# Performance work log

Measured on AMD Instinct MI355X. Metric: run time of the kernel, lower is better.

The kernel has to match this reference:

```python
import jax, jax.numpy as jnp
import numpy as np

VOCAB = 100000
PAD_ID = VOCAB - 2
INTEREST_ID = VOCAB - 1


def setup_inputs() -> dict:
    key = jax.random.key(0)
    k1, k2, k3 = jax.random.split(key, 3)
    B, S, H = 1024, 200, 128
    hidden_states = jax.random.normal(k1, (B, S, H), dtype=jnp.float32)
    input_ids = jax.random.randint(k2, (B, S), 0, VOCAB, dtype=jnp.int64)
    w_proj = jax.random.normal(k3, (H,), dtype=jnp.float32) * (1.0 / np.sqrt(H))
    b_proj = jnp.zeros((1,), dtype=jnp.float32)
    return {"hidden_states": hidden_states, "input_ids": input_ids,
            "w_proj": w_proj, "b_proj": b_proj}


def reference(hidden_states, input_ids, w_proj, b_proj):
    # hidden_states: [B, S, H]; input_ids: [B, S]
    B, S, H = hidden_states.shape
    mask = (input_ids != PAD_ID) & (input_ids != INTEREST_ID)  # [B, S]
    # additive attention: queries = hidden, keys = first token state
    keys = hidden_states[:, 0:1, :]                 # [B, 1, H]
    features = jnp.tanh(hidden_states + keys)       # [B, S, H]
    scores = jnp.einsum('bsh,h->bs', features, w_proj) + b_proj[0]
    scores = jnp.where(mask, scores, -jnp.inf)
    attention_weights = jax.nn.softmax(scores, axis=-1)  # [B, S]
    # scatter-add attention weights into vocab-sized output (duplicate ids accumulate)
    batch_idx = jnp.arange(B)[:, None]              # [B, 1]
    repeat_probs = jnp.zeros((B, VOCAB), dtype=hidden_states.dtype)
    repeat_probs = repeat_probs.at[batch_idx, input_ids].add(attention_weights)
    return repeat_probs
```

## Files before the change

### kernel.cpp

```cpp
#include <hip/hip_runtime.h>
#include <math.h>

#define B_          1024
#define S_          200
#define H_          128
#define VOCAB_      100000
#define PAD_ID_     99998
#define INTEREST_ID_ 99999

__global__ __launch_bounds__(256) void repeat_decoder_kernel(
    const float* __restrict__ hs,
    const int*   __restrict__ ids,
    const float* __restrict__ w,
    const float* __restrict__ bp,
    float*       __restrict__ out)
{
    __shared__ float s_scores[S_];
    __shared__ float s_red[8];

    const int batch = blockIdx.x;
    const int tid   = threadIdx.x;
    const int wave  = tid >> 6;
    const int lane  = tid & 63;

    const float* hsb = hs + (size_t)batch * (S_ * H_);

    const float2 key = ((const float2*)hsb)[lane];
    const float2 wv  = ((const float2*)w)[lane];

    for (int s = wave; s < S_; s += 4) {
        const float2 x = ((const float2*)(hsb + s * H_))[lane];
        float acc = tanhf(x.x + key.x) * wv.x + tanhf(x.y + key.y) * wv.y;
        #pragma unroll
        for (int off = 32; off; off >>= 1)
            acc += __shfl_down(acc, off, 64);
        if (lane == 0) s_scores[s] = acc;
    }
    __syncthreads();

    const float bias = bp[0];
    int   id    = 0;
    bool  valid = false;
    float sc    = -INFINITY;
    if (tid < S_) {
        id    = ids[batch * S_ + tid];
        valid = (id != PAD_ID_) && (id != INTEREST_ID_);
        sc    = valid ? (s_scores[tid] + bias) : -INFINITY;
    }

    float m = sc;
    #pragma unroll
    for (int off = 32; off; off >>= 1)
        m = fmaxf(m, __shfl_down(m, off, 64));
    if (lane == 0) s_red[wave] = m;
    __syncthreads();
    m = fmaxf(fmaxf(s_red[0], s_red[1]), fmaxf(s_red[2], s_red[3]));

    const float e = (tid < S_ && valid) ? expf(sc - m) : 0.0f;
    float t = e;
    #pragma unroll
    for (int off = 32; off; off >>= 1)
        t += __shfl_down(t, off, 64);
    if (lane == 0) s_red[4 + wave] = t;
    __syncthreads();
    const float sum = s_red[4] + s_red[5] + s_red[6] + s_red[7];

    if (tid < S_ && valid) {
        atomicAdd(&out[(size_t)batch * VOCAB_ + id], e / sum);
    }
}

extern "C" void kernel_launch(void* const* d_in, const int* in_sizes, int n_in,
                              void* d_out, int out_size, void* d_ws, size_t ws_size,
                              hipStream_t stream) {
    const float* hs  = (const float*)d_in[0];
    const int*   ids = (const int*)d_in[1];
    const float* w   = (const float*)d_in[2];
    const float* bp  = (const float*)d_in[3];
    float*       out = (float*)d_out;

    hipMemsetAsync(d_out, 0, (size_t)out_size * sizeof(float), stream);

    repeat_decoder_kernel<<<B_, 256, 0, stream>>>(hs, ids, w, bp, out);
}
```

Baseline: 511.0 us.

## Fuse output zeroing into decoder kernel and widen to 512 threads with float4 loads

```diff
diff --git a/kernel.cpp b/kernel.cpp
--- a/kernel.cpp
+++ b/kernel.cpp
@@ -1,14 +1,15 @@
 #include <hip/hip_runtime.h>
 #include <math.h>
 
-#define B_          1024
-#define S_          200
-#define H_          128
-#define VOCAB_      100000
-#define PAD_ID_     99998
+#define B_           1024
+#define S_           200
+#define H_           128
+#define VOCAB_       100000
+#define PAD_ID_      99998
 #define INTEREST_ID_ 99999
+#define NTHREADS_    512
 
-__global__ __launch_bounds__(256) void repeat_decoder_kernel(
+__global__ __launch_bounds__(NTHREADS_) void repeat_decoder_fused(
     const float* __restrict__ hs,
     const int*   __restrict__ ids,
     const float* __restrict__ w,
@@ -16,26 +17,42 @@
     float*       __restrict__ out)
 {
     __shared__ float s_scores[S_];
-    __shared__ float s_red[8];
+    __shared__ float s_red[16];
 
     const int batch = blockIdx.x;
     const int tid   = threadIdx.x;
     const int wave  = tid >> 6;
     const int lane  = tid & 63;
+    const int half  = lane >> 5;
+    const int hl    = lane & 31;
 
-    const float* hsb = hs + (size_t)batch * (S_ * H_);
+    const float* hsb  = hs + (size_t)batch * (S_ * H_);
+    float*       rowo = out + (size_t)batch * VOCAB_;
 
-    const float2 key = ((const float2*)hsb)[lane];
-    const float2 wv  = ((const float2*)w)[lane];
+    const float4 key = ((const float4*)hsb)[hl];
+    const float4 wv  = ((const float4*)w)[hl];
 
-    for (int s = wave; s < S_; s += 4) {
-        const float2 x = ((const float2*)(hsb + s * H_))[lane];
-        float acc = tanhf(x.x + key.x) * wv.x + tanhf(x.y + key.y) * wv.y;
+    for (int s0 = wave * 2; s0 < S_; s0 += 16) {
+        const int s = s0 + half;
+        const float4 x = ((const float4*)(hsb + s * H_))[hl];
+        float acc = tanhf(x.x + key.x) * wv.x
+                  + tanhf(x.y + key.y) * wv.y
+                  + tanhf(x.z + key.z) * wv.z
+                  + tanhf(x.w + key.w) * wv.w;
         #pragma unroll
-        for (int off = 32; off; off >>= 1)
-            acc += __shfl_down(acc, off, 64);
-        if (lane == 0) s_scores[s] = acc;
+        for (int off = 16; off; off >>= 1)
+            acc += __shfl_xor(acc, off, 64);
+        if (hl == 0) s_scores[s] = acc;
     }
+
+    {
+        float4* rowo4 = (float4*)rowo;
+        const float4 z = make_float4(0.f, 0.f, 0.f, 0.f);
+        #pragma unroll 4
+        for (int i = tid; i < VOCAB_ / 4; i += NTHREADS_)
+            rowo4[i] = z;
+    }
+
     __syncthreads();
 
     const float bias = bp[0];
@@ -54,19 +71,21 @@
         m = fmaxf(m, __shfl_down(m, off, 64));
     if (lane == 0) s_red[wave] = m;
     __syncthreads();
-    m = fmaxf(fmaxf(s_red[0], s_red[1]), fmaxf(s_red[2], s_red[3]));
+    m = fmaxf(fmaxf(fmaxf(s_red[0], s_red[1]), fmaxf(s_red[2], s_red[3])),
+              fmaxf(fmaxf(s_red[4], s_red[5]), fmaxf(s_red[6], s_red[7])));
 
-    const float e = (tid < S_ && valid) ? expf(sc - m) : 0.0f;
+    const float e = valid ? expf(sc - m) : 0.0f;
     float t = e;
     #pragma unroll
     for (int off = 32; off; off >>= 1)
         t += __shfl_down(t, off, 64);
-    if (lane == 0) s_red[4 + wave] = t;
+    if (lane == 0) s_red[8 + wave] = t;
     __syncthreads();
-    const float sum = s_red[4] + s_red[5] + s_red[6] + s_red[7];
+    const float sum = (s_red[8]  + s_red[9])  + (s_red[10] + s_red[11])
+                    + (s_red[12] + s_red[13]) + (s_red[14] + s_red[15]);
 
-    if (tid < S_ && valid) {
-        atomicAdd(&out[(size_t)batch * VOCAB_ + id], e / sum);
+    if (valid) {
+        atomicAdd(&rowo[id], e / sum);
     }
 }
 
@@ -79,7 +98,5 @@
     const float* bp  = (const float*)d_in[3];
     float*       out = (float*)d_out;
 
-    hipMemsetAsync(d_out, 0, (size_t)out_size * sizeof(float), stream);
-
-    repeat_decoder_kernel<<<B_, 256, 0, stream>>>(hs, ids, w, bp, out);
+    repeat_decoder_fused<<<B_, NTHREADS_, 0, stream>>>(hs, ids, w, bp, out);
 }
```

Measured after the change: 496.3 us. 1.03x faster.
